# Performance work log

Hardware: AMD Instinct MI355X
Metric: run time of the kernel (lower is better)

The kernel has to match this reference:

```python
import jax, jax.numpy as jnp
import numpy as np

B, L, S, D, H, CTX = 2, 2048, 512, 1024, 16, 1024
HD = D // H
HID = 4 * D
EPS = 1e-6


def _ln(x):
    mu = jnp.mean(x, axis=-1, keepdims=True)
    var = jnp.mean((x - mu) ** 2, axis=-1, keepdims=True)
    return (x - mu) * jax.lax.rsqrt(var + EPS)


def _rotate_half(x):
    x1, x2 = jnp.split(x, 2, axis=-1)
    return jnp.concatenate([-x2, x1], axis=-1)


def _heads(t):  # [B,N,D] -> [B,H,N,HD]
    return t.reshape(t.shape[0], t.shape[1], H, HD).transpose(0, 2, 1, 3)


def _merge(t):  # [B,H,N,HD] -> [B,N,D]
    return t.transpose(0, 2, 1, 3).reshape(t.shape[0], t.shape[2], D)


def setup_inputs() -> dict:
    key = jax.random.key(0)
    ks = jax.random.split(key, 24)
    s = 0.02
    inp = {
        "x": jax.random.normal(ks[0], (B, L, D), jnp.float32),
        "timestep_emb": jax.random.normal(ks[1], (B, D), jnp.float32),
        "context_emb": jax.random.normal(ks[2], (B, S, CTX), jnp.float32),
        "rope_emb": jax.random.normal(ks[3], (L, HD), jnp.float32),
        # adaLN modulation: Linear(D -> 6D) with bias
        "w_mod": jax.random.normal(ks[4], (D, 6 * D), jnp.float32) * s,
        "b_mod": jnp.zeros((6 * D,), jnp.float32),
        # self-attention (no qkv bias, out has bias)
        "wq_s": jax.random.normal(ks[5], (D, D), jnp.float32) * s,
        "wk_s": jax.random.normal(ks[6], (D, D), jnp.float32) * s,
        "wv_s": jax.random.normal(ks[7], (D, D), jnp.float32) * s,
        "wo_s": jax.random.normal(ks[8], (D, D), jnp.float32) * s,
        "bo_s": jnp.zeros((D,), jnp.float32),
        # cross-attention (q/k/v no bias, out has bias)
        "wq_c": jax.random.normal(ks[9], (D, D), jnp.float32) * s,
        "wk_c": jax.random.normal(ks[10], (CTX, D), jnp.float32) * s,
        "wv_c": jax.random.normal(ks[11], (CTX, D), jnp.float32) * s,
        "wo_c": jax.random.normal(ks[12], (D, D), jnp.float32) * s,
        "bo_c": jnp.zeros((D,), jnp.float32),
        # MLP
        "w1": jax.random.normal(ks[13], (D, HID), jnp.float32) * s,
        "b1": jnp.zeros((HID,), jnp.float32),
        "w2": jax.random.normal(ks[14], (HID, D), jnp.float32) * s,
        "b2": jnp.zeros((D,), jnp.float32),
    }
    return inp


def reference(x, timestep_emb, context_emb, rope_emb,
              w_mod, b_mod,
              wq_s, wk_s, wv_s, wo_s, bo_s,
              wq_c, wk_c, wv_c, wo_c, bo_c,
              w1, b1, w2, b2):
    scale = HD ** -0.5
    # adaLN modulation from timestep embedding
    mods = jnp.split(timestep_emb @ w_mod + b_mod, 6, axis=-1)
    shift_msa, scale_msa, gate_msa, shift_mlp, scale_mlp, gate_mlp = mods

    # --- self-attention with RoPE ---
    nx = _ln(x) * (1.0 + scale_msa[:, None, :]) + shift_msa[:, None, :]
    q = _heads(nx @ wq_s)
    k = _heads(nx @ wk_s)
    v = _heads(nx @ wv_s)
    cos = jnp.cos(rope_emb)[None, None]  # [1,1,L,HD]
    sin = jnp.sin(rope_emb)[None, None]
    q = q * cos + _rotate_half(q) * sin
    k = k * cos + _rotate_half(k) * sin
    attn = jax.nn.softmax(jnp.einsum("bhqd,bhkd->bhqk", q, k) * scale, axis=-1)
    sa = _merge(jnp.einsum("bhqk,bhkd->bhqd", attn, v)) @ wo_s + bo_s
    x = x + gate_msa[:, None, :] * sa

    # --- cross-attention (no mask) ---
    nx = _ln(x)
    q = _heads(nx @ wq_c)
    k = _heads(context_emb @ wk_c)
    v = _heads(context_emb @ wv_c)
    attn = jax.nn.softmax(jnp.einsum("bhqd,bhkd->bhqk", q, k) * scale, axis=-1)
    ca = _merge(jnp.einsum("bhqk,bhkd->bhqd", attn, v)) @ wo_c + bo_c
    x = x + ca

    # --- MLP with modulation + gate ---
    nx = _ln(x) * (1.0 + scale_mlp[:, None, :]) + shift_mlp[:, None, :]
    h = jax.nn.gelu(nx @ w1 + b1, approximate=False)
    x = x + gate_mlp[:, None, :] * (h @ w2 + b2)
    return x
```

## Files before the change

### kernel.cpp

```cpp
#include <hip/hip_runtime.h>
#include <hip/hip_bf16.h>


typedef short short8 __attribute__((ext_vector_type(8)));
typedef float f32x4 __attribute__((ext_vector_type(4)));
typedef float f32x16 __attribute__((ext_vector_type(16)));

#define DEV __device__ __forceinline__

DEV unsigned short f2b(float f) {
  __hip_bfloat16 h = __float2bfloat16(f);
  return *reinterpret_cast<unsigned short*>(&h);
}
DEV float b2f(unsigned short u) {
  unsigned int x = ((unsigned int)u) << 16;
  return __builtin_bit_cast(float, x);
}
DEV unsigned int pk2(float lo, float hi) {
  unsigned int r;
  asm("v_cvt_pk_bf16_f32 %0, %1, %2" : "=v"(r) : "v"(lo), "v"(hi));
  return r;
}
DEV void vpsw(unsigned int& a, unsigned int& b) {
  asm("v_permlane32_swap_b32 %0, %1" : "+v"(a), "+v"(b));
}

#define GLB(p) ((const __attribute__((address_space(1))) void*)(p))
#define LDSP(p) ((__attribute__((address_space(3))) void*)(p))

__global__ __launch_bounds__(256) void transpose_cast(
    const float* __restrict__ in, unsigned short* __restrict__ out, int R, int C,
    float scale) {
  __shared__ float tile[32][33];
  int bx = blockIdx.x * 32, by = blockIdx.y * 32;
  int tx = threadIdx.x, ty = threadIdx.y;
#pragma unroll
  for (int i = ty; i < 32; i += 8)
    tile[i][tx] = in[(size_t)(by + i) * C + bx + tx];
  __syncthreads();
#pragma unroll
  for (int i = ty; i < 32; i += 8)
    out[(size_t)(bx + i) * R + by + tx] = f2b(tile[tx][i] * scale);
}

__global__ __launch_bounds__(256) void cast_bf16(
    const float* __restrict__ in, unsigned short* __restrict__ out, int n) {
  int i = blockIdx.x * 256 + threadIdx.x;
  if (i < n) out[i] = f2b(in[i]);
}

__global__ __launch_bounds__(256) void rope_tab(
    const float* __restrict__ rope, float* __restrict__ cosT, float* __restrict__ sinT, int n) {
  int i = blockIdx.x * 256 + threadIdx.x;
  if (i < n) {
    float v = rope[i];
    cosT[i] = cosf(v);
    sinT[i] = sinf(v);
  }
}

__global__ __launch_bounds__(256) void mods_kernel(
    const float* __restrict__ te, const unsigned short* __restrict__ wmodT,
    const float* __restrict__ bmod, float* __restrict__ mods) {
  int w = blockIdx.x * 4 + (threadIdx.x >> 6);
  int lane = threadIdx.x & 63;
  int b = w / 6144, j = w % 6144;
  const unsigned short* wr = wmodT + (size_t)j * 1024;
  const float* ter = te + (size_t)b * 1024;
  int k0 = lane * 16;
  float sum = 0.f;
#pragma unroll
  for (int u = 0; u < 2; ++u) {
    short8 wv = *(const short8*)(wr + k0 + u * 8);
#pragma unroll
    for (int e = 0; e < 8; ++e)
      sum += b2f((unsigned short)wv[e]) * ter[k0 + u * 8 + e];
  }
#pragma unroll
  for (int off = 32; off >= 1; off >>= 1) sum += __shfl_down(sum, off);
  if (lane == 0) mods[(size_t)b * 6144 + j] = sum + bmod[j];
}

__global__ __launch_bounds__(256) void ln_mod(
    const float* __restrict__ x, const float* __restrict__ mods,
    unsigned short* __restrict__ out, int scale_ofs, int shift_ofs) {
  int row = blockIdx.x;
  int b = row >> 11;
  int tid = threadIdx.x;
  const float* xr = x + (size_t)row * 1024;
  float4 v = ((const float4*)xr)[tid];
  float s = v.x + v.y + v.z + v.w;
  float ss = v.x * v.x + v.y * v.y + v.z * v.z + v.w * v.w;
#pragma unroll
  for (int off = 32; off >= 1; off >>= 1) {
    s += __shfl_down(s, off);
    ss += __shfl_down(ss, off);
  }
  __shared__ float red[8];
  int wave = tid >> 6, lane = tid & 63;
  if (lane == 0) { red[wave] = s; red[4 + wave] = ss; }
  __syncthreads();
  if (tid == 0) {
    float S = red[0] + red[1] + red[2] + red[3];
    float SS = red[4] + red[5] + red[6] + red[7];
    float mu = S * (1.f / 1024.f);
    red[0] = mu;
    red[1] = SS * (1.f / 1024.f) - mu * mu;
  }
  __syncthreads();
  float mu = red[0];
  float rs = rsqrtf(red[1] + 1e-6f);
  float vv[4] = {v.x, v.y, v.z, v.w};
  unsigned short o[4];
#pragma unroll
  for (int c = 0; c < 4; ++c) {
    int col = tid * 4 + c;
    float nv = (vv[c] - mu) * rs;
    if (scale_ofs >= 0)
      nv = nv * (1.f + mods[(size_t)b * 6144 + scale_ofs + col]) +
           mods[(size_t)b * 6144 + shift_ofs + col];
    o[c] = f2b(nv);
  }
  *(ushort4*)(&out[(size_t)row * 1024 + tid * 4]) = *(const ushort4*)o;
}

__global__ __launch_bounds__(256) void rope_apply(
    unsigned short* __restrict__ qb, unsigned short* __restrict__ kb,
    const float* __restrict__ cosT, const float* __restrict__ sinT) {
  int idx = blockIdx.x * 256 + threadIdx.x;
  unsigned short* buf = blockIdx.y ? kb : qb;
  int row = idx >> 9;
  int rem = idx & 511;
  int h = rem >> 5, d = rem & 31;
  int l = row & 2047;
  size_t base = (size_t)row * 1024 + h * 64 + d;
  float x1 = b2f(buf[base]), x2 = b2f(buf[base + 32]);
  float c1 = cosT[l * 64 + d], s1 = sinT[l * 64 + d];
  float c2 = cosT[l * 64 + d + 32], s2 = sinT[l * 64 + d + 32];
  buf[base] = f2b(x1 * c1 - x2 * s1);
  buf[base + 32] = f2b(x2 * c2 + x1 * s2);
}

template <int EPI, int MI, int NJ>
DEV void gemm_epilogue(f32x4 (&acc)[MI][NJ], void* Cout, const float* bias,
                       const float* mods, int gate_ofs, const float* src,
                       int N, int rowsPerB, int m0, int n0, int wm, int wn,
                       int g, int r) {
#pragma unroll
  for (int i = 0; i < MI; ++i) {
#pragma unroll
    for (int j = 0; j < NJ; ++j) {
#pragma unroll
      for (int q = 0; q < 4; ++q) {
        size_t grow = (size_t)(m0 + wm + i * 16 + g * 4 + q);
        size_t gcol = (size_t)(n0 + wn + j * 16 + r);
        float v = acc[i][j][q];
        if constexpr (EPI == 0) {
          ((unsigned short*)Cout)[grow * N + gcol] = f2b(v);
        } else if constexpr (EPI == 1) {
          v += bias[gcol];
          float ge = 0.5f * v * (1.0f + erff(v * 0.70710678f));
          ((unsigned short*)Cout)[grow * N + gcol] = f2b(ge);
        } else if constexpr (EPI == 3) {
          size_t buf = gcol >> 10;
          ((unsigned short*)Cout)[buf * (4096ull * 1024) + grow * 1024 + (gcol & 1023)] = f2b(v);
        } else {
          v += bias[gcol];
          float gate = 1.0f;
          if (gate_ofs >= 0)
            gate = mods[(grow / rowsPerB) * 6144 + gate_ofs + gcol];
          ((float*)Cout)[grow * N + gcol] = src[grow * N + gcol] + gate * v;
        }
      }
    }
  }
}

template <int EPI>
__global__ __launch_bounds__(256, 2) void gemm_bt(
    const unsigned short* __restrict__ A, const unsigned short* __restrict__ Bt,
    void* __restrict__ Cout, const float* __restrict__ bias,
    const float* __restrict__ mods, int gate_ofs, const float* __restrict__ src,
    int M, int N, int K, int rowsPerB) {
  __shared__ unsigned short As[128 * 32];
  __shared__ unsigned short Bs[128 * 32];
  const int tid = threadIdx.x;
  const int wave = tid >> 6, lane = tid & 63;
  const int g = lane >> 4, r = lane & 15;
  const int m0 = blockIdx.y * 128, n0 = blockIdx.x * 128;
  const int wm = (wave >> 1) * 64, wn = (wave & 1) * 64;
  const int srow = lane >> 2;
  const int scol = (lane & 3) * 8;

  f32x4 acc[4][4] = {};

  for (int k0 = 0; k0 < K; k0 += 32) {
    __syncthreads();
#pragma unroll
    for (int cc = 0; cc < 4; ++cc) {
      int c = wave * 4 + cc;
      int isB = c >> 3;
      int cl = c & 7;
      int row = cl * 16 + srow;
      const unsigned short* gsrc =
          isB ? (Bt + (size_t)(n0 + row) * K + k0 + scol)
              : (A + (size_t)(m0 + row) * K + k0 + scol);
      unsigned short* ldst = (isB ? Bs : As) + cl * 512;
      __builtin_amdgcn_global_load_lds(GLB(gsrc), LDSP(ldst), 16, 0, 0);
    }
    __syncthreads();

    short8 bfr[4];
#pragma unroll
    for (int j = 0; j < 4; ++j)
      bfr[j] = *(const short8*)(&Bs[(wn + j * 16 + r) * 32 + g * 8]);
#pragma unroll
    for (int i = 0; i < 4; ++i) {
      short8 af = *(const short8*)(&As[(wm + i * 16 + r) * 32 + g * 8]);
#pragma unroll
      for (int j = 0; j < 4; ++j)
        acc[i][j] = __builtin_amdgcn_mfma_f32_16x16x32_bf16(af, bfr[j], acc[i][j], 0, 0, 0);
    }
  }
  gemm_epilogue<EPI, 4, 4>(acc, Cout, bias, mods, gate_ofs, src, N, rowsPerB,
                           m0, n0, wm, wn, g, r);
}

template <int EPI>
__global__ __launch_bounds__(256) void gemm_pipe(
    const unsigned short* __restrict__ A, const unsigned short* __restrict__ Bt,
    void* __restrict__ Cout, const float* __restrict__ bias,
    const float* __restrict__ mods, int gate_ofs, const float* __restrict__ src,
    int M, int N, int K, int rowsPerB, int mshift) {
  __shared__ unsigned short lds[4 * 16384];
  const int tid = threadIdx.x;
  const int wave = tid >> 6, lane = tid & 63;
  const int g = lane >> 4, r = lane & 15;
  const int flat = blockIdx.x;
  const int xcd = flat & 7, idx = flat >> 3;
  const int mt = xcd * (1 << mshift) + (idx & ((1 << mshift) - 1));
  const int nt = idx >> mshift;
  const int m0 = mt * 128, n0 = nt * 128;
  const int wm = (wave >> 1) * 64, wn = (wave & 1) * 64;
  const int srow8 = lane >> 3;
  const int sck = (lane & 7) ^ srow8;

  f32x4 acc[4][4] = {};

  auto stage = [&](int t, int bufi) {
    const int k0 = t * 64;
#pragma unroll
    for (int i = 0; i < 8; ++i) {
      int u = wave * 8 + i;
      int isB = u >> 4;
      int uu = u & 15;
      int rl = uu * 8 + srow8;
      const unsigned short* gsrc =
          (isB ? (Bt + (size_t)(n0 + rl) * K) : (A + (size_t)(m0 + rl) * K)) +
          k0 + sck * 8;
      unsigned short* dst = (unsigned short*)lds + bufi * 16384 + isB * 8192 + uu * 512;
      __builtin_amdgcn_global_load_lds(GLB(gsrc), LDSP(dst), 16, 0, 0);
    }
  };

  const int nt_k = K / 64;
  stage(0, 0);
  stage(1, 1);
  stage(2, 2);

  for (int t = 0; t < nt_k; ++t) {
    int rem = nt_k - t;
    if (rem >= 3) {
      asm volatile("s_waitcnt vmcnt(16)" ::: "memory");
    } else if (rem == 2) {
      asm volatile("s_waitcnt vmcnt(8)" ::: "memory");
    } else {
      asm volatile("s_waitcnt vmcnt(0)" ::: "memory");
    }
    __builtin_amdgcn_sched_barrier(0);
    __builtin_amdgcn_s_barrier();
    __builtin_amdgcn_sched_barrier(0);
    if (t + 3 < nt_k) stage(t + 3, (t + 3) & 3);

    const unsigned short* Ab = (const unsigned short*)lds + (t & 3) * 16384;
    const unsigned short* Bb = Ab + 8192;
#pragma unroll
    for (int ks = 0; ks < 2; ++ks) {
      short8 bfr[4];
#pragma unroll
      for (int j = 0; j < 4; ++j) {
        int row = wn + j * 16 + r;
        bfr[j] = *(const short8*)&Bb[row * 64 + ((g + ks * 4) ^ (r & 7)) * 8];
      }
#pragma unroll
      for (int i = 0; i < 4; ++i) {
        int row = wm + i * 16 + r;
        short8 af = *(const short8*)&Ab[row * 64 + ((g + ks * 4) ^ (r & 7)) * 8];
#pragma unroll
        for (int j = 0; j < 4; ++j)
          acc[i][j] = __builtin_amdgcn_mfma_f32_16x16x32_bf16(af, bfr[j], acc[i][j], 0, 0, 0);
      }
    }
  }
  gemm_epilogue<EPI, 4, 4>(acc, Cout, bias, mods, gate_ofs, src, N, rowsPerB,
                           m0, n0, wm, wn, g, r);
}

template <int EPI>
__global__ __launch_bounds__(256) void gemm_p2(
    const unsigned short* __restrict__ A, const unsigned short* __restrict__ Bt,
    void* __restrict__ Cout, const float* __restrict__ bias,
    const float* __restrict__ mods, int gate_ofs, const float* __restrict__ src,
    int M, int N, int K, int rowsPerB, int ntn) {
  __shared__ unsigned short lds[3 * 12288];
  const int tid = threadIdx.x;
  const int wave = tid >> 6, lane = tid & 63;
  const int g = lane >> 4, r = lane & 15;
  const int flat = blockIdx.x;
  const int nt = flat % ntn, mt = flat / ntn;
  const int m0 = mt * 64, n0 = nt * 128;
  const int wm = (wave >> 1) * 32, wn = (wave & 1) * 64;
  const int srow8 = lane >> 3;
  const int sck = (lane & 7) ^ srow8;

  f32x4 acc[2][4] = {};

  auto stage = [&](int t, int bufi) {
    const int k0 = t * 64;
    unsigned short* base = (unsigned short*)lds + bufi * 12288;
#pragma unroll
    for (int i = 0; i < 2; ++i) {
      int u = wave * 2 + i;
      int rl = u * 8 + srow8;
      const unsigned short* gsrc = A + (size_t)(m0 + rl) * K + k0 + sck * 8;
      __builtin_amdgcn_global_load_lds(GLB(gsrc), LDSP(base + u * 512), 16, 0, 0);
    }
#pragma unroll
    for (int i = 0; i < 4; ++i) {
      int u = wave * 4 + i;
      int rl = u * 8 + srow8;
      const unsigned short* gsrc = Bt + (size_t)(n0 + rl) * K + k0 + sck * 8;
      __builtin_amdgcn_global_load_lds(GLB(gsrc), LDSP(base + 4096 + u * 512), 16, 0, 0);
    }
  };

  const int ntk = K / 64;
  stage(0, 0);
  stage(1, 1);
  int cbuf = 0, sbuf = 2;

  for (int t = 0; t < ntk; ++t) {
    if (t < ntk - 1) {
      asm volatile("s_waitcnt vmcnt(6)" ::: "memory");
    } else {
      asm volatile("s_waitcnt vmcnt(0)" ::: "memory");
    }
    __builtin_amdgcn_sched_barrier(0);
    __builtin_amdgcn_s_barrier();
    __builtin_amdgcn_sched_barrier(0);
    if (t + 2 < ntk) {
      stage(t + 2, sbuf);
      sbuf = (sbuf == 2) ? 0 : sbuf + 1;
    }

    const unsigned short* Ab = (const unsigned short*)lds + cbuf * 12288;
    const unsigned short* Bb = Ab + 4096;
#pragma unroll
    for (int ks = 0; ks < 2; ++ks) {
      short8 bfr[4];
#pragma unroll
      for (int j = 0; j < 4; ++j) {
        int row = wn + j * 16 + r;
        bfr[j] = *(const short8*)&Bb[row * 64 + ((g + ks * 4) ^ (r & 7)) * 8];
      }
#pragma unroll
      for (int i = 0; i < 2; ++i) {
        int row = wm + i * 16 + r;
        short8 af = *(const short8*)&Ab[row * 64 + ((g + ks * 4) ^ (r & 7)) * 8];
#pragma unroll
        for (int j = 0; j < 4; ++j)
          acc[i][j] = __builtin_amdgcn_mfma_f32_16x16x32_bf16(af, bfr[j], acc[i][j], 0, 0, 0);
      }
    }
    cbuf = (cbuf == 2) ? 0 : cbuf + 1;
  }
  gemm_epilogue<EPI, 2, 4>(acc, Cout, bias, mods, gate_ofs, src, N, rowsPerB,
                           m0, n0, wm, wn, g, r);
}

__global__ __launch_bounds__(256, 2) void flash2(
    const unsigned short* __restrict__ Q, const unsigned short* __restrict__ Kv,
    const unsigned short* __restrict__ Vv, unsigned short* __restrict__ O,
    int Lk) {
  __shared__ unsigned short lds[16384];
  const int tid = threadIdx.x, wave = tid >> 6, lane = tid & 63;
  const int hi = lane >> 5, lq = lane & 31;
  const int flat = blockIdx.x;
  const int xcd = flat & 7, rr = flat >> 3;
  const int gl = rr >> 4, qt = rr & 15;
  const int g = xcd * 4 + gl;
  const int h = g & 15, b = g >> 4;
  const int Lq = 2048, D = 1024;

  const unsigned short* Qbase =
      Q + ((size_t)b * Lq + qt * 128 + wave * 32 + lq) * D + h * 64;
  const unsigned short* Kbase = Kv + (size_t)b * Lk * D + h * 64;
  const unsigned short* Vbase = Vv + (size_t)b * Lk * D + h * 64;

  short8 qf[4];
#pragma unroll
  for (int kb = 0; kb < 4; ++kb)
    qf[kb] = *(const short8*)(Qbase + kb * 16 + hi * 8);

  const short8 ones = {0x3F80, 0x3F80, 0x3F80, 0x3F80, 0x3F80, 0x3F80, 0x3F80, 0x3F80};

  const int kr0 = tid >> 3, kc0 = tid & 7;
  const int kvp = tid >> 3, db = tid & 7;
  const int kch0 = (kc0 ^ (kr0 & 7) ^ (kr0 >> 3)) & 7;
  const int kch1 = kch0 ^ 4;
  const int f0 = (lq & 7) ^ (lq >> 3);
  const int swz0 = f0 << 4, swz1 = swz0 ^ 64;

  int vby[8];
#pragma unroll
  for (int e = 0; e < 8; ++e) {
    int d = db * 8 + e;
    vby[e] = d * 128 + ((kvp * 4) ^ (((e ^ db) & 7) << 4));
  }

  float m_run = -3.0e38f;
  f32x16 o0 = {}, o1 = {}, lacc = {};
  short8 vr0, vr1;

  {
    const unsigned short* v0 = Vbase + (size_t)(2 * kvp) * D + db * 8;
    vr0 = *(const short8*)v0;
    vr1 = *(const short8*)(v0 + D);
    const unsigned short* s0 = Kbase + (size_t)kr0 * D + kch0 * 8;
    const unsigned short* s1 = Kbase + (size_t)(kr0 + 32) * D + kch1 * 8;
    __builtin_amdgcn_global_load_lds(GLB(s0), LDSP(&lds[wave * 512]), 16, 0, 0);
    __builtin_amdgcn_global_load_lds(GLB(s1), LDSP(&lds[2048 + wave * 512]), 16, 0, 0);
    char* vt = (char*)&lds[8192];
#pragma unroll
    for (int e = 0; e < 8; ++e)
      *(unsigned int*)(vt + vby[e]) =
          (unsigned int)(unsigned short)vr0[e] |
          ((unsigned int)(unsigned short)vr1[e] << 16);
  }
  __syncthreads();

  const int nkt = Lk / 64;
  int cb = 0;
  for (int kt = 0; kt < nkt; ++kt) {
    const bool pf = (kt + 1 < nkt);
    if (pf) {
      const unsigned short* v0 = Vbase + (size_t)((kt + 1) * 64 + 2 * kvp) * D + db * 8;
      vr0 = *(const short8*)v0;
      vr1 = *(const short8*)(v0 + D);
      const int nb = (cb ^ 1) * 4096;
      const unsigned short* s0 = Kbase + (size_t)((kt + 1) * 64 + kr0) * D + kch0 * 8;
      const unsigned short* s1 = Kbase + (size_t)((kt + 1) * 64 + kr0 + 32) * D + kch1 * 8;
      __builtin_amdgcn_global_load_lds(GLB(s0), LDSP(&lds[nb + wave * 512]), 16, 0, 0);
      __builtin_amdgcn_global_load_lds(GLB(s1), LDSP(&lds[nb + 2048 + wave * 512]), 16, 0, 0);
    }

    f32x16 s0a = {}, s1a = {};
    {
      const unsigned short* K0 = &lds[cb * 4096];
      __builtin_amdgcn_s_setprio(1);
#pragma unroll
      for (int ks = 0; ks < 4; ++ks) {
        int lo = ks * 32 + hi * 16;
        short8 a0 = *(const short8*)&K0[lq * 64 + ((lo ^ swz0) >> 1)];
        short8 a1 = *(const short8*)&K0[(32 + lq) * 64 + ((lo ^ swz1) >> 1)];
        s0a = __builtin_amdgcn_mfma_f32_32x32x16_bf16(a0, qf[ks], s0a, 0, 0, 0);
        s1a = __builtin_amdgcn_mfma_f32_32x32x16_bf16(a1, qf[ks], s1a, 0, 0, 0);
      }
      __builtin_amdgcn_s_setprio(0);
    }

    float tm[8];
#pragma unroll
    for (int i = 0; i < 8; ++i)
      tm[i] = fmaxf(fmaxf(s0a[i], s0a[i + 8]), fmaxf(s1a[i], s1a[i + 8]));
    float pm = fmaxf(fmaxf(fmaxf(tm[0], tm[1]), fmaxf(tm[2], tm[3])),
                     fmaxf(fmaxf(tm[4], tm[5]), fmaxf(tm[6], tm[7])));
    {
      unsigned int ua = __builtin_bit_cast(unsigned int, pm), ub = ua;
      vpsw(ua, ub);
      pm = fmaxf(__builtin_bit_cast(float, ua), __builtin_bit_cast(float, ub));
    }
    if (__any(pm - m_run > 8.0f)) {
      float mnew = fmaxf(m_run, pm);
      float alpha = exp2f(m_run - mnew);
      lacc[0] *= alpha;
#pragma unroll
      for (int i = 0; i < 16; ++i) { o0[i] *= alpha; o1[i] *= alpha; }
      m_run = mnew;
    }
    float mc = m_run;
#pragma unroll
    for (int i = 0; i < 16; ++i) s0a[i] = exp2f(s0a[i] - mc);
#pragma unroll
    for (int i = 0; i < 16; ++i) s1a[i] = exp2f(s1a[i] - mc);

    short8 pbf[4];
#pragma unroll
    for (int kb = 0; kb < 4; ++kb) {
      int bb = (kb & 1) * 8;
      float p0, p1, p2, p3, p4, p5, p6, p7;
      if (kb < 2) {
        p0 = s0a[bb + 0]; p1 = s0a[bb + 1]; p2 = s0a[bb + 2]; p3 = s0a[bb + 3];
        p4 = s0a[bb + 4]; p5 = s0a[bb + 5]; p6 = s0a[bb + 6]; p7 = s0a[bb + 7];
      } else {
        p0 = s1a[bb + 0]; p1 = s1a[bb + 1]; p2 = s1a[bb + 2]; p3 = s1a[bb + 3];
        p4 = s1a[bb + 4]; p5 = s1a[bb + 5]; p6 = s1a[bb + 6]; p7 = s1a[bb + 7];
      }
      unsigned int u0 = pk2(p0, p1), u1 = pk2(p2, p3);
      unsigned int u2 = pk2(p4, p5), u3 = pk2(p6, p7);
      vpsw(u0, u2);
      vpsw(u1, u3);
      union { unsigned int u[4]; short8 s; } fr;
      fr.u[0] = u0; fr.u[1] = u1; fr.u[2] = u2; fr.u[3] = u3;
      pbf[kb] = fr.s;
    }

    if (pf) {
      char* vt = (char*)&lds[8192 + (cb ^ 1) * 4096];
#pragma unroll
      for (int e = 0; e < 8; ++e)
        *(unsigned int*)(vt + vby[e]) =
            (unsigned int)(unsigned short)vr0[e] |
            ((unsigned int)(unsigned short)vr1[e] << 16);
    }

    {
      const unsigned short* V0 = &lds[8192 + cb * 4096];
      __builtin_amdgcn_s_setprio(1);
#pragma unroll
      for (int kb = 0; kb < 4; ++kb) {
        int lo = kb * 32 + hi * 16;
        short8 vf0 = *(const short8*)&V0[lq * 64 + ((lo ^ swz0) >> 1)];
        short8 vf1 = *(const short8*)&V0[(32 + lq) * 64 + ((lo ^ swz1) >> 1)];
        o0 = __builtin_amdgcn_mfma_f32_32x32x16_bf16(vf0, pbf[kb], o0, 0, 0, 0);
        o1 = __builtin_amdgcn_mfma_f32_32x32x16_bf16(vf1, pbf[kb], o1, 0, 0, 0);
        lacc = __builtin_amdgcn_mfma_f32_32x32x16_bf16(ones, pbf[kb], lacc, 0, 0, 0);
      }
      __builtin_amdgcn_s_setprio(0);
    }

    __syncthreads();
    cb ^= 1;
  }

  __syncthreads();
  float rl = 1.0f / lacc[0];
  unsigned short* os = &lds[wave * 2048];
#pragma unroll
  for (int t = 0; t < 2; ++t) {
#pragma unroll
    for (int c = 0; c < 4; ++c) {
      int dbase = 32 * t + 8 * c + 4 * hi;
      float v0 = (t ? o1[4 * c + 0] : o0[4 * c + 0]) * rl;
      float v1 = (t ? o1[4 * c + 1] : o0[4 * c + 1]) * rl;
      float v2 = (t ? o1[4 * c + 2] : o0[4 * c + 2]) * rl;
      float v3 = (t ? o1[4 * c + 3] : o0[4 * c + 3]) * rl;
      int by0 = lq * 128 + ((dbase * 2) ^ ((lq & 7) << 4));
      int by1 = lq * 128 + (((dbase + 2) * 2) ^ ((lq & 7) << 4));
      *(unsigned int*)((char*)os + by0) = pk2(v0, v1);
      *(unsigned int*)((char*)os + by1) = pk2(v2, v3);
    }
  }
  int q2 = lane >> 1;
  unsigned short* orow =
      O + ((size_t)b * Lq + qt * 128 + wave * 32 + q2) * D + h * 64;
#pragma unroll
  for (int j = 0; j < 4; ++j) {
    int j2 = (lane & 1) * 4 + j;
    int byr = q2 * 128 + ((j2 * 16) ^ ((q2 & 7) << 4));
    short8 vv = *(const short8*)((char*)os + byr);
    *(short8*)(orow + j2 * 8) = vv;
  }
}

extern "C" void kernel_launch(void* const* d_in, const int* in_sizes, int n_in,
                              void* d_out, int out_size, void* d_ws, size_t ws_size,
                              hipStream_t stream) {
  (void)in_sizes; (void)n_in; (void)out_size; (void)ws_size;
  const float* x_in = (const float*)d_in[0];
  const float* te   = (const float*)d_in[1];
  const float* ctx  = (const float*)d_in[2];
  const float* rope = (const float*)d_in[3];
  const float* wmod = (const float*)d_in[4];
  const float* bmod = (const float*)d_in[5];
  const float* wqs  = (const float*)d_in[6];
  const float* wks  = (const float*)d_in[7];
  const float* wvs  = (const float*)d_in[8];
  const float* wos  = (const float*)d_in[9];
  const float* bos  = (const float*)d_in[10];
  const float* wqc  = (const float*)d_in[11];
  const float* wkc  = (const float*)d_in[12];
  const float* wvc  = (const float*)d_in[13];
  const float* woc  = (const float*)d_in[14];
  const float* boc  = (const float*)d_in[15];
  const float* w1   = (const float*)d_in[16];
  const float* b1   = (const float*)d_in[17];
  const float* w2   = (const float*)d_in[18];
  const float* b2   = (const float*)d_in[19];
  float* out = (float*)d_out;

  char* w = (char*)d_ws;
  size_t o = 0;
  auto alloc = [&](size_t bytes) {
    char* p = w + o;
    o = (o + bytes + 255) & ~(size_t)255;
    return p;
  };
  unsigned short* wmodT = (unsigned short*)alloc(6144ull * 1024 * 2);
  unsigned short* wqsT  = (unsigned short*)alloc(1024ull * 1024 * 2);
  unsigned short* wksT  = (unsigned short*)alloc(1024ull * 1024 * 2);
  unsigned short* wvsT  = (unsigned short*)alloc(1024ull * 1024 * 2);
  unsigned short* wosT  = (unsigned short*)alloc(1024ull * 1024 * 2);
  unsigned short* wqcT  = (unsigned short*)alloc(1024ull * 1024 * 2);
  unsigned short* wkcT  = (unsigned short*)alloc(1024ull * 1024 * 2);
  unsigned short* wvcT  = (unsigned short*)alloc(1024ull * 1024 * 2);
  unsigned short* wocT  = (unsigned short*)alloc(1024ull * 1024 * 2);
  unsigned short* w1T   = (unsigned short*)alloc(4096ull * 1024 * 2);
  unsigned short* w2T   = (unsigned short*)alloc(1024ull * 4096 * 2);
  float* modsb = (float*)alloc(2ull * 6144 * 4);
  float* cosT  = (float*)alloc(2048ull * 64 * 4);
  float* sinT  = (float*)alloc(2048ull * 64 * 4);
  unsigned short* nx   = (unsigned short*)alloc(4096ull * 1024 * 2);
  unsigned short* ctxb = (unsigned short*)alloc(1024ull * 1024 * 2);
  unsigned short* qb = (unsigned short*)alloc(4096ull * 1024 * 2);
  unsigned short* kb = (unsigned short*)alloc(4096ull * 1024 * 2);
  unsigned short* vb = (unsigned short*)alloc(4096ull * 1024 * 2);
  unsigned short* ao = (unsigned short*)alloc(4096ull * 1024 * 2);
  float* xw = (float*)alloc(4096ull * 1024 * 4);
  unsigned short* hbuf = qb;

  const float c1 = 0.125f * 1.4426950408889634f;

  dim3 tb(32, 8);
  transpose_cast<<<dim3(6144 / 32, 1024 / 32), tb, 0, stream>>>(wmod, wmodT, 1024, 6144, 1.0f);
  transpose_cast<<<dim3(32, 32), tb, 0, stream>>>(wqs, wqsT, 1024, 1024, c1);
  transpose_cast<<<dim3(32, 32), tb, 0, stream>>>(wks, wksT, 1024, 1024, 1.0f);
  transpose_cast<<<dim3(32, 32), tb, 0, stream>>>(wvs, wvsT, 1024, 1024, 1.0f);
  transpose_cast<<<dim3(32, 32), tb, 0, stream>>>(wos, wosT, 1024, 1024, 1.0f);
  transpose_cast<<<dim3(32, 32), tb, 0, stream>>>(wqc, wqcT, 1024, 1024, 1.0f);
  transpose_cast<<<dim3(32, 32), tb, 0, stream>>>(wkc, wkcT, 1024, 1024, c1);
  transpose_cast<<<dim3(32, 32), tb, 0, stream>>>(wvc, wvcT, 1024, 1024, 1.0f);
  transpose_cast<<<dim3(32, 32), tb, 0, stream>>>(woc, wocT, 1024, 1024, 1.0f);
  transpose_cast<<<dim3(4096 / 32, 1024 / 32), tb, 0, stream>>>(w1, w1T, 1024, 4096, 1.0f);
  transpose_cast<<<dim3(1024 / 32, 4096 / 32), tb, 0, stream>>>(w2, w2T, 4096, 1024, 1.0f);

  cast_bf16<<<4096, 256, 0, stream>>>(ctx, ctxb, 1024 * 1024);
  rope_tab<<<512, 256, 0, stream>>>(rope, cosT, sinT, 2048 * 64);
  mods_kernel<<<3072, 256, 0, stream>>>(te, wmodT, bmod, modsb);

  ln_mod<<<4096, 256, 0, stream>>>(x_in, modsb, nx, 1024, 0);
  gemm_pipe<3><<<768, 256, 0, stream>>>(nx, wqsT, qb, nullptr, nullptr, -1, nullptr, 4096, 3072, 1024, 2048, 2);
  rope_apply<<<dim3(8192, 2), 256, 0, stream>>>(qb, kb, cosT, sinT);
  flash2<<<512, 256, 0, stream>>>(qb, kb, vb, ao, 2048);
  gemm_p2<2><<<512, 256, 0, stream>>>(ao, wosT, xw, bos, modsb, 2048, x_in, 4096, 1024, 1024, 2048, 8);

  ln_mod<<<4096, 256, 0, stream>>>(xw, modsb, nx, -1, -1);
  gemm_p2<0><<<512, 256, 0, stream>>>(nx, wqcT, qb, nullptr, nullptr, -1, nullptr, 4096, 1024, 1024, 2048, 8);
  gemm_p2<3><<<256, 256, 0, stream>>>(ctxb, wkcT, kb, nullptr, nullptr, -1, nullptr, 1024, 2048, 1024, 512, 16);
  flash2<<<512, 256, 0, stream>>>(qb, kb, vb, ao, 512);
  gemm_p2<2><<<512, 256, 0, stream>>>(ao, wocT, xw, boc, modsb, -1, xw, 4096, 1024, 1024, 2048, 8);

  ln_mod<<<4096, 256, 0, stream>>>(xw, modsb, nx, 4096, 3072);
  gemm_bt<1><<<dim3(32, 32), 256, 0, stream>>>(nx, w1T, hbuf, b1, nullptr, -1, nullptr, 4096, 4096, 1024, 2048);
  gemm_p2<2><<<512, 256, 0, stream>>>(hbuf, w2T, out, b2, modsb, 5120, xw, 4096, 1024, 4096, 2048, 8);
}
```

Measured before the change: 420.8 us.

## Software-pipeline flash attention QK with softmax/PV and batch weight transposes

Result: faster. 409.9 us (-2.6%).

```diff
diff --git a/kernel.cpp b/kernel.cpp
--- a/kernel.cpp
+++ b/kernel.cpp
@@ -23,6 +23,11 @@
 }
 DEV void vpsw(unsigned int& a, unsigned int& b) {
   asm("v_permlane32_swap_b32 %0, %1" : "+v"(a), "+v"(b));
+}
+DEV float max3f(float a, float b, float c) {
+  float r;
+  asm("v_max3_f32 %0, %1, %2, %3" : "=v"(r) : "v"(a), "v"(b), "v"(c));
+  return r;
 }
 
 #define GLB(p) ((const __attribute__((address_space(1))) void*)(p))
@@ -41,6 +46,24 @@
 #pragma unroll
   for (int i = ty; i < 32; i += 8)
     out[(size_t)(bx + i) * R + by + tx] = f2b(tile[tx][i] * scale);
+}
+
+struct TCB { const float* in; unsigned short* out; float scale; };
+struct TC8 { TCB m[8]; };
+__global__ __launch_bounds__(256) void transpose_cast8(TC8 a) {
+  __shared__ float tile[32][33];
+  const float* in = a.m[blockIdx.z].in;
+  unsigned short* out = a.m[blockIdx.z].out;
+  float scale = a.m[blockIdx.z].scale;
+  int bx = blockIdx.x * 32, by = blockIdx.y * 32;
+  int tx = threadIdx.x, ty = threadIdx.y;
+#pragma unroll
+  for (int i = ty; i < 32; i += 8)
+    tile[i][tx] = in[(size_t)(by + i) * 1024 + bx + tx];
+  __syncthreads();
+#pragma unroll
+  for (int i = ty; i < 32; i += 8)
+    out[(size_t)(bx + i) * 1024 + by + tx] = f2b(tile[tx][i] * scale);
 }
 
 __global__ __launch_bounds__(256) void cast_bf16(
@@ -392,7 +415,7 @@
     const unsigned short* __restrict__ Q, const unsigned short* __restrict__ Kv,
     const unsigned short* __restrict__ Vv, unsigned short* __restrict__ O,
     int Lk) {
-  __shared__ unsigned short lds[16384];
+  __shared__ unsigned short lds[20480];
   const int tid = threadIdx.x, wave = tid >> 6, lane = tid & 63;
   const int hi = lane >> 5, lq = lane & 31;
   const int flat = blockIdx.x;
@@ -431,60 +454,46 @@
   float m_run = -3.0e38f;
   f32x16 o0 = {}, o1 = {}, lacc = {};
   short8 vr0, vr1;
-
-  {
-    const unsigned short* v0 = Vbase + (size_t)(2 * kvp) * D + db * 8;
+  short8 pbf[4];
+
+  auto stageK = [&](int t, int bi) {
+    const unsigned short* s0 = Kbase + (size_t)(t * 64 + kr0) * D + kch0 * 8;
+    const unsigned short* s1 = Kbase + (size_t)(t * 64 + kr0 + 32) * D + kch1 * 8;
+    __builtin_amdgcn_global_load_lds(GLB(s0), LDSP(&lds[bi * 4096 + wave * 512]), 16, 0, 0);
+    __builtin_amdgcn_global_load_lds(GLB(s1), LDSP(&lds[bi * 4096 + 2048 + wave * 512]), 16, 0, 0);
+  };
+  auto loadV = [&](int t) {
+    const unsigned short* v0 = Vbase + (size_t)(t * 64 + 2 * kvp) * D + db * 8;
     vr0 = *(const short8*)v0;
     vr1 = *(const short8*)(v0 + D);
-    const unsigned short* s0 = Kbase + (size_t)kr0 * D + kch0 * 8;
-    const unsigned short* s1 = Kbase + (size_t)(kr0 + 32) * D + kch1 * 8;
-    __builtin_amdgcn_global_load_lds(GLB(s0), LDSP(&lds[wave * 512]), 16, 0, 0);
-    __builtin_amdgcn_global_load_lds(GLB(s1), LDSP(&lds[2048 + wave * 512]), 16, 0, 0);
-    char* vt = (char*)&lds[8192];
+  };
+  auto writeV = [&](int t) {
+    char* vt = (char*)&lds[12288 + (t & 1) * 4096];
 #pragma unroll
     for (int e = 0; e < 8; ++e)
       *(unsigned int*)(vt + vby[e]) =
           (unsigned int)(unsigned short)vr0[e] |
           ((unsigned int)(unsigned short)vr1[e] << 16);
-  }
-  __syncthreads();
-
-  const int nkt = Lk / 64;
-  int cb = 0;
-  for (int kt = 0; kt < nkt; ++kt) {
-    const bool pf = (kt + 1 < nkt);
-    if (pf) {
-      const unsigned short* v0 = Vbase + (size_t)((kt + 1) * 64 + 2 * kvp) * D + db * 8;
-      vr0 = *(const short8*)v0;
-      vr1 = *(const short8*)(v0 + D);
-      const int nb = (cb ^ 1) * 4096;
-      const unsigned short* s0 = Kbase + (size_t)((kt + 1) * 64 + kr0) * D + kch0 * 8;
-      const unsigned short* s1 = Kbase + (size_t)((kt + 1) * 64 + kr0 + 32) * D + kch1 * 8;
-      __builtin_amdgcn_global_load_lds(GLB(s0), LDSP(&lds[nb + wave * 512]), 16, 0, 0);
-      __builtin_amdgcn_global_load_lds(GLB(s1), LDSP(&lds[nb + 2048 + wave * 512]), 16, 0, 0);
-    }
-
-    f32x16 s0a = {}, s1a = {};
-    {
-      const unsigned short* K0 = &lds[cb * 4096];
-      __builtin_amdgcn_s_setprio(1);
-#pragma unroll
-      for (int ks = 0; ks < 4; ++ks) {
-        int lo = ks * 32 + hi * 16;
-        short8 a0 = *(const short8*)&K0[lq * 64 + ((lo ^ swz0) >> 1)];
-        short8 a1 = *(const short8*)&K0[(32 + lq) * 64 + ((lo ^ swz1) >> 1)];
-        s0a = __builtin_amdgcn_mfma_f32_32x32x16_bf16(a0, qf[ks], s0a, 0, 0, 0);
-        s1a = __builtin_amdgcn_mfma_f32_32x32x16_bf16(a1, qf[ks], s1a, 0, 0, 0);
-      }
-      __builtin_amdgcn_s_setprio(0);
-    }
-
+  };
+  auto qk = [&](int bi, f32x16& sa0, f32x16& sa1) {
+    const unsigned short* K0 = &lds[bi * 4096];
+#pragma unroll
+    for (int ks = 0; ks < 4; ++ks) {
+      int lo = ks * 32 + hi * 16;
+      short8 a0 = *(const short8*)&K0[lq * 64 + ((lo ^ swz0) >> 1)];
+      short8 a1 = *(const short8*)&K0[(32 + lq) * 64 + ((lo ^ swz1) >> 1)];
+      sa0 = __builtin_amdgcn_mfma_f32_32x32x16_bf16(a0, qf[ks], sa0, 0, 0, 0);
+      sa1 = __builtin_amdgcn_mfma_f32_32x32x16_bf16(a1, qf[ks], sa1, 0, 0, 0);
+    }
+  };
+  auto finish = [&](f32x16& s0a, f32x16& s1a) {
     float tm[8];
 #pragma unroll
     for (int i = 0; i < 8; ++i)
-      tm[i] = fmaxf(fmaxf(s0a[i], s0a[i + 8]), fmaxf(s1a[i], s1a[i + 8]));
-    float pm = fmaxf(fmaxf(fmaxf(tm[0], tm[1]), fmaxf(tm[2], tm[3])),
-                     fmaxf(fmaxf(tm[4], tm[5]), fmaxf(tm[6], tm[7])));
+      tm[i] = fmaxf(max3f(s0a[i], s0a[i + 8], s1a[i]), s1a[i + 8]);
+    float x = max3f(tm[0], tm[1], tm[2]);
+    float y = max3f(tm[3], tm[4], tm[5]);
+    float pm = fmaxf(max3f(tm[6], tm[7], x), y);
     {
       unsigned int ua = __builtin_bit_cast(unsigned int, pm), ub = ua;
       vpsw(ua, ub);
@@ -503,8 +512,6 @@
     for (int i = 0; i < 16; ++i) s0a[i] = exp2f(s0a[i] - mc);
 #pragma unroll
     for (int i = 0; i < 16; ++i) s1a[i] = exp2f(s1a[i] - mc);
-
-    short8 pbf[4];
 #pragma unroll
     for (int kb = 0; kb < 4; ++kb) {
       int bb = (kb & 1) * 8;
@@ -524,36 +531,52 @@
       fr.u[0] = u0; fr.u[1] = u1; fr.u[2] = u2; fr.u[3] = u3;
       pbf[kb] = fr.s;
     }
-
-    if (pf) {
-      char* vt = (char*)&lds[8192 + (cb ^ 1) * 4096];
-#pragma unroll
-      for (int e = 0; e < 8; ++e)
-        *(unsigned int*)(vt + vby[e]) =
-            (unsigned int)(unsigned short)vr0[e] |
-            ((unsigned int)(unsigned short)vr1[e] << 16);
-    }
-
-    {
-      const unsigned short* V0 = &lds[8192 + cb * 4096];
-      __builtin_amdgcn_s_setprio(1);
-#pragma unroll
-      for (int kb = 0; kb < 4; ++kb) {
-        int lo = kb * 32 + hi * 16;
-        short8 vf0 = *(const short8*)&V0[lq * 64 + ((lo ^ swz0) >> 1)];
-        short8 vf1 = *(const short8*)&V0[(32 + lq) * 64 + ((lo ^ swz1) >> 1)];
-        o0 = __builtin_amdgcn_mfma_f32_32x32x16_bf16(vf0, pbf[kb], o0, 0, 0, 0);
-        o1 = __builtin_amdgcn_mfma_f32_32x32x16_bf16(vf1, pbf[kb], o1, 0, 0, 0);
-        lacc = __builtin_amdgcn_mfma_f32_32x32x16_bf16(ones, pbf[kb], lacc, 0, 0, 0);
-      }
-      __builtin_amdgcn_s_setprio(0);
-    }
-
+  };
+  auto pv = [&](int t) {
+    const unsigned short* V0 = &lds[12288 + (t & 1) * 4096];
+    __builtin_amdgcn_s_setprio(1);
+#pragma unroll
+    for (int kb = 0; kb < 4; ++kb) {
+      int lo = kb * 32 + hi * 16;
+      short8 vf0 = *(const short8*)&V0[lq * 64 + ((lo ^ swz0) >> 1)];
+      short8 vf1 = *(const short8*)&V0[(32 + lq) * 64 + ((lo ^ swz1) >> 1)];
+      o0 = __builtin_amdgcn_mfma_f32_32x32x16_bf16(vf0, pbf[kb], o0, 0, 0, 0);
+      o1 = __builtin_amdgcn_mfma_f32_32x32x16_bf16(vf1, pbf[kb], o1, 0, 0, 0);
+      lacc = __builtin_amdgcn_mfma_f32_32x32x16_bf16(ones, pbf[kb], lacc, 0, 0, 0);
+    }
+    __builtin_amdgcn_s_setprio(0);
+  };
+
+  const int nkt = Lk / 64;
+
+  stageK(0, 0);
+  loadV(0);
+  writeV(0);
+  stageK(1, 1);
+  __syncthreads();
+
+  f32x16 sA0 = {}, sA1 = {}, sB0, sB1;
+  qk(0, sA0, sA1);
+
+  auto pstep = [&](int t, f32x16& n0, f32x16& n1, f32x16& p0, f32x16& p1) {
+    const int tq = t + 1;
+    if (tq < nkt) {
+      loadV(tq);
+      if (tq + 1 < nkt) stageK(tq + 1, (tq + 1) % 3);
+      n0 = {}; n1 = {};
+      qk(tq % 3, n0, n1);
+    }
+    finish(p0, p1);
+    if (tq < nkt) writeV(tq);
+    pv(t);
     __syncthreads();
-    cb ^= 1;
-  }
-
-  __syncthreads();
+  };
+
+  for (int t = 0; t < nkt; t += 2) {
+    pstep(t, sB0, sB1, sA0, sA1);
+    pstep(t + 1, sA0, sA1, sB0, sB1);
+  }
+
   float rl = 1.0f / lacc[0];
   unsigned short* os = &lds[wave * 2048];
 #pragma unroll
@@ -643,14 +666,16 @@
 
   dim3 tb(32, 8);
   transpose_cast<<<dim3(6144 / 32, 1024 / 32), tb, 0, stream>>>(wmod, wmodT, 1024, 6144, 1.0f);
-  transpose_cast<<<dim3(32, 32), tb, 0, stream>>>(wqs, wqsT, 1024, 1024, c1);
-  transpose_cast<<<dim3(32, 32), tb, 0, stream>>>(wks, wksT, 1024, 1024, 1.0f);
-  transpose_cast<<<dim3(32, 32), tb, 0, stream>>>(wvs, wvsT, 1024, 1024, 1.0f);
-  transpose_cast<<<dim3(32, 32), tb, 0, stream>>>(wos, wosT, 1024, 1024, 1.0f);
-  transpose_cast<<<dim3(32, 32), tb, 0, stream>>>(wqc, wqcT, 1024, 1024, 1.0f);
-  transpose_cast<<<dim3(32, 32), tb, 0, stream>>>(wkc, wkcT, 1024, 1024, c1);
-  transpose_cast<<<dim3(32, 32), tb, 0, stream>>>(wvc, wvcT, 1024, 1024, 1.0f);
-  transpose_cast<<<dim3(32, 32), tb, 0, stream>>>(woc, wocT, 1024, 1024, 1.0f);
+  TC8 tc8;
+  tc8.m[0] = {wqs, wqsT, c1};
+  tc8.m[1] = {wks, wksT, 1.0f};
+  tc8.m[2] = {wvs, wvsT, 1.0f};
+  tc8.m[3] = {wos, wosT, 1.0f};
+  tc8.m[4] = {wqc, wqcT, 1.0f};
+  tc8.m[5] = {wkc, wkcT, c1};
+  tc8.m[6] = {wvc, wvcT, 1.0f};
+  tc8.m[7] = {woc, wocT, 1.0f};
+  transpose_cast8<<<dim3(32, 32, 8), tb, 0, stream>>>(tc8);
   transpose_cast<<<dim3(4096 / 32, 1024 / 32), tb, 0, stream>>>(w1, w1T, 1024, 4096, 1.0f);
   transpose_cast<<<dim3(1024 / 32, 4096 / 32), tb, 0, stream>>>(w2, w2T, 4096, 1024, 1.0f);
 
```
